# Kernel tuning notes

Measured on AMD Instinct MI355X. Metric: run time of the kernel, lower is better.

The kernel has to match this reference:

```python
import jax, jax.numpy as jnp
import numpy as np

EPS = 1e-5
SLOPE = 0.2


def _conv3d(x, w, stride):
    # x: [B, Cin, D, H, W], w: [Cout, Cin, 3, 3, 3]
    return jax.lax.conv_general_dilated(
        x, w, window_strides=(stride, stride, stride),
        padding=[(1, 1), (1, 1), (1, 1)],
        dimension_numbers=("NCDHW", "OIDHW", "NCDHW"))


def _layernorm_c(y, g, b):
    # LayerNorm over the channel (feature) dim, matching nn.LayerNorm(C) on [N, C]
    mu = jnp.mean(y, axis=1, keepdims=True)
    var = jnp.mean((y - mu) ** 2, axis=1, keepdims=True)
    yn = (y - mu) * jax.lax.rsqrt(var + EPS)
    return yn * g[None, :, None, None, None] + b[None, :, None, None, None]


def _leaky(y):
    return jnp.where(y > 0, y, SLOPE * y)


def _block(x, m, w, g, b, stride):
    # x already zero at inactive sites, so dense conv == sparse gather-scatter conv
    y = _conv3d(x, w, stride)
    if stride > 1:
        # strided SparseConv3d: output active iff any input in 3x3x3 window active
        ones_k = jnp.ones((1, 1, 3, 3, 3), x.dtype)
        m = (_conv3d(m, ones_k, stride) > 0).astype(x.dtype)
    y = _leaky(_layernorm_c(y, g, b))
    return y * m, m


def setup_inputs() -> dict:
    key = jax.random.key(0)
    ks = jax.random.split(key, 16)
    B, D = 2, 64
    x = jax.random.normal(ks[0], (B, 3, D, D, D), jnp.float32)
    mask = jax.random.randint(ks[1], (B, D, D, D), 0, 2) > 0
    chans = [(3, 64), (64, 128), (128, 256), (256, 512)]
    inp = {"x": x, "mask": mask}
    for i, (ci, co) in enumerate(chans):
        inp[f"w{i+1}"] = jax.random.normal(ks[2 + 3 * i], (co, ci, 3, 3, 3), jnp.float32) * 0.05
        inp[f"g{i+1}"] = jnp.ones((co,), jnp.float32)
        inp[f"b{i+1}"] = jnp.zeros((co,), jnp.float32)
    return inp


def reference(x, mask, w1, g1, b1, w2, g2, b2, w3, g3, b3, w4, g4, b4):
    m = mask.astype(x.dtype)[:, None]          # [B,1,D,H,W]
    x = x * m                                  # zero inactive sites
    # SubMConv3d: active set unchanged (stride 1)
    y, m = _block(x, m, w1, g1, b1, 1)
    y, m = _block(y, m, w2, g2, b2, 2)
    y, m = _block(y, m, w3, g3, b3, 2)
    y, m = _block(y, m, w4, g4, b4, 2)
    # .dense() fills inactive sites with 0 (already the case), then amax over D,H,W
    return jnp.max(y, axis=(2, 3, 4))          # [B, 512]
```

## Files before the change

kernel.cpp:

```cpp
#include <hip/hip_runtime.h>
#include <hip/hip_bf16.h>
#include <stdint.h>

#define EPS 1e-5f
#define SLOPE 0.2f

typedef __attribute__((ext_vector_type(8))) short short8;
typedef __attribute__((ext_vector_type(4))) float f32x4;

static __device__ inline ushort f2bf(float f) {
  __hip_bfloat16 h = __float2bfloat16(f);
  return *reinterpret_cast<ushort*>(&h);
}

static __device__ inline short8 u4_to_s8(uint a, uint b, uint c, uint d) {
  union { uint4 u; short8 s; } cv;
  cv.u.x = a; cv.u.y = b; cv.u.z = c; cv.u.w = d;
  return cv.s;
}

__global__ void mask_detect_k(const uint8_t* __restrict__ raw, int nbytes,
                              unsigned* __restrict__ flag) {
  unsigned local = 0;
  for (int i = blockIdx.x * blockDim.x + threadIdx.x; i < nbytes;
       i += gridDim.x * blockDim.x)
    if (i & 3) local |= raw[i];
  if (local) atomicOr(flag, 1u);
}

__global__ void xclm_k(const float* __restrict__ x, const uint8_t* __restrict__ raw,
                       const unsigned* __restrict__ flag,
                       uint8_t* __restrict__ m1, ushort* __restrict__ xclp) {
  int id = blockIdx.x * blockDim.x + threadIdx.x;
  if (id >= 2 * 262144) return;
  uint8_t v;
  if (*flag) {
    v = raw[id];
  } else {
    size_t j = 4 * (size_t)id;
    v = (uint8_t)(raw[j] | raw[j + 1] | raw[j + 2] | raw[j + 3]);
  }
  v = v ? 1 : 0;
  m1[id] = v;
  float mk = (float)v;
  int b  = id >> 18;
  int sp = id & 262143;
  int xx = sp & 63, yy = (sp >> 6) & 63, zz = sp >> 12;
  size_t base = (size_t)b * 3 * 262144 + sp;
  float x0 = x[base] * mk;
  float x1 = x[base + 262144] * mk;
  float x2 = x[base + 2 * 262144] * mk;
  uint2 u;
  u.x = ((uint)f2bf(x1) << 16) | (uint)f2bf(x0);
  u.y = (uint)f2bf(x2);
  size_t pidx = ((((size_t)(b * 66 + zz + 1)) * 66 + (yy + 1)) * 66 + (xx + 1)) * 4;
  *reinterpret_cast<uint2*>(xclp + pidx) = u;
}

__global__ void mask_down_k(const uint8_t* __restrict__ mi,
                            uint8_t* __restrict__ mo, int DIN) {
  int W = DIN >> 1;
  int id = blockIdx.x * blockDim.x + threadIdx.x;
  int total = 2 * W * W * W;
  if (id >= total) return;
  int xo = id % W; int t = id / W;
  int yo = t % W;  t /= W;
  int zo = t % W;  int b = t / W;
  int any = 0;
  for (int dz = 0; dz < 3; ++dz) {
    int z = 2 * zo + dz - 1; if (z < 0 || z >= DIN) continue;
    for (int dy = 0; dy < 3; ++dy) {
      int y = 2 * yo + dy - 1; if (y < 0 || y >= DIN) continue;
      for (int dx = 0; dx < 3; ++dx) {
        int x = 2 * xo + dx - 1; if (x < 0 || x >= DIN) continue;
        any |= mi[(((size_t)b * DIN + z) * DIN + y) * DIN + x];
      }
    }
  }
  mo[id] = any ? 1 : 0;
}

__global__ void wprep_k(const float* __restrict__ w1, const float* __restrict__ w2,
                        const float* __restrict__ w3, const float* __restrict__ w4,
                        ushort* __restrict__ wb1, ushort* __restrict__ wb2,
                        ushort* __restrict__ wb3, ushort* __restrict__ wb4) {
  int id = blockIdx.x * blockDim.x + threadIdx.x;
  if (id < 8192) {
    int k = id & 127, c = id >> 7;
    int tap = k >> 2, ci = k & 3;
    float v = (tap < 27 && ci < 3) ? w1[c * 81 + ci * 27 + tap] : 0.f;
    wb1[id] = f2bf(v);
    return;
  }
  id -= 8192;
  if (id < 128 * 1728) {
    int kn = id % 1728, c = id / 1728;
    int off = kn >> 6, ci = kn & 63;
    wb2[(size_t)c * 1728 + kn] = f2bf(w2[(size_t)c * 1728 + ci * 27 + off]);
    return;
  }
  id -= 128 * 1728;
  if (id < 256 * 3456) {
    int kn = id % 3456, c = id / 3456;
    int off = kn >> 7, ci = kn & 127;
    wb3[(size_t)c * 3456 + kn] = f2bf(w3[(size_t)c * 3456 + ci * 27 + off]);
    return;
  }
  id -= 256 * 3456;
  if (id < 512 * 6912) {
    int kn = id % 6912, c = id / 6912;
    int off = kn >> 8, ci = kn & 255;
    wb4[(size_t)c * 6912 + kn] = f2bf(w4[(size_t)c * 6912 + ci * 27 + off]);
  }
}

__global__ __launch_bounds__(256) void conv1_gemm(
    const ushort* __restrict__ xclp,
    const ushort* __restrict__ wb1,
    const float* __restrict__ gamma,
    const float* __restrict__ beta,
    const uint8_t* __restrict__ msk,
    ushort* __restrict__ out)
{
  const int t    = threadIdx.x;
  const int lane = t & 63;
  const int wave = t >> 6;
  const int c8   = lane >> 4;

  const int bid = blockIdx.x;
  const int yp = bid & 31;
  const int zq = (bid >> 5) & 15;
  const int b  = bid >> 9;
  const int y0 = yp * 2;
  const int z0 = zq * 4;

  __shared__ uint2 tile[1584];

  const uint2* xin = reinterpret_cast<const uint2*>(xclp);
  const long gbase = (((long)(b * 66 + z0)) * 66 + y0) * 66;
  for (int e = t; e < 1584; e += 256) {
    int p = e / 264;
    tile[e] = xin[gbase + e + p * 4092];
  }

  int eoff[2][2][2];
#pragma unroll
  for (int kb = 0; kb < 2; ++kb)
#pragma unroll
    for (int kh = 0; kh < 2; ++kh)
#pragma unroll
      for (int p = 0; p < 2; ++p) {
        int tap = kb * 16 + kh * 8 + c8 * 2 + p;
        int off = 0;
        if (tap < 27) {
          int dz = tap / 9, rr = tap - dz * 9;
          int dy = rr / 3, dx = rr - dy * 3;
          off = dz * 264 + dy * 66 + dx;
        }
        eoff[kb][kh][p] = off;
      }

  int ebase[2];
#pragma unroll
  for (int nf = 0; nf < 2; ++nf) {
    int nl = wave * 32 + nf * 16 + (lane & 15);
    ebase[nf] = (nl >> 6) * 66 + (nl & 63);
  }

  float gr[4][4], br_[4][4];
#pragma unroll
  for (int mf = 0; mf < 4; ++mf) {
    int cb = mf * 16 + c8 * 4;
    f32x4 gv  = *reinterpret_cast<const f32x4*>(gamma + cb);
    f32x4 bv2 = *reinterpret_cast<const f32x4*>(beta + cb);
#pragma unroll
    for (int r = 0; r < 4; ++r) { gr[mf][r] = gv[r]; br_[mf][r] = bv2[r]; }
  }

  __syncthreads();

  for (int zi = 0; zi < 4; ++zi) {
    const int zsh = zi * 264;
    f32x4 acc[4][2];
#pragma unroll
    for (int i = 0; i < 4; ++i)
#pragma unroll
      for (int j = 0; j < 2; ++j) acc[i][j] = (f32x4)(0.f);

#pragma unroll
    for (int kb = 0; kb < 2; ++kb) {
      short8 afr[4][2];
#pragma unroll
      for (int mf = 0; mf < 4; ++mf)
#pragma unroll
        for (int kh = 0; kh < 2; ++kh) {
          int row = mf * 16 + (lane & 15);
          int k   = kb * 64 + (c8 + kh * 4) * 8;
          afr[mf][kh] = *reinterpret_cast<const short8*>(wb1 + row * 128 + k);
        }
#pragma unroll
      for (int nf = 0; nf < 2; ++nf)
#pragma unroll
        for (int kh = 0; kh < 2; ++kh) {
          uint2 v0 = tile[ebase[nf] + zsh + eoff[kb][kh][0]];
          uint2 v1 = tile[ebase[nf] + zsh + eoff[kb][kh][1]];
          short8 bfr = u4_to_s8(v0.x, v0.y, v1.x, v1.y);
#pragma unroll
          for (int mf = 0; mf < 4; ++mf)
            acc[mf][nf] = __builtin_amdgcn_mfma_f32_16x16x32_bf16(
                afr[mf][kh], bfr, acc[mf][nf], 0, 0, 0);
        }
    }

    const int z = z0 + zi;
    const int voxbase = ((b * 64 + z) * 64 + y0) * 64;
#pragma unroll
    for (int nf = 0; nf < 2; ++nf) {
      float s = 0.f, sq = 0.f;
#pragma unroll
      for (int mf = 0; mf < 4; ++mf)
#pragma unroll
        for (int r = 0; r < 4; ++r) {
          float v = acc[mf][nf][r];
          s += v; sq += v * v;
        }
      s  += __shfl_xor(s, 16);  sq += __shfl_xor(sq, 16);
      s  += __shfl_xor(s, 32);  sq += __shfl_xor(sq, 32);
      const float mean = s * (1.f / 64.f);
      const float var  = sq * (1.f / 64.f) - mean * mean;
      const float rstd = rsqrtf(var + EPS);
      const int vox = voxbase + wave * 32 + nf * 16 + (lane & 15);
      const float mk = msk[vox] ? 1.f : 0.f;
#pragma unroll
      for (int mf = 0; mf < 4; ++mf) {
        uint2 u;
        float r0 = (acc[mf][nf][0] - mean) * rstd * gr[mf][0] + br_[mf][0];
        float r1 = (acc[mf][nf][1] - mean) * rstd * gr[mf][1] + br_[mf][1];
        float r2 = (acc[mf][nf][2] - mean) * rstd * gr[mf][2] + br_[mf][2];
        float r3 = (acc[mf][nf][3] - mean) * rstd * gr[mf][3] + br_[mf][3];
        r0 = (r0 > 0.f ? r0 : SLOPE * r0) * mk;
        r1 = (r1 > 0.f ? r1 : SLOPE * r1) * mk;
        r2 = (r2 > 0.f ? r2 : SLOPE * r2) * mk;
        r3 = (r3 > 0.f ? r3 : SLOPE * r3) * mk;
        u.x = ((uint)f2bf(r1) << 16) | (uint)f2bf(r0);
        u.y = ((uint)f2bf(r3) << 16) | (uint)f2bf(r2);
        *reinterpret_cast<uint2*>(out + (size_t)vox * 64 + mf * 16 + c8 * 4) = u;
      }
    }
  }
}

__global__ __launch_bounds__(256) void conv2_gemm(
    const ushort* __restrict__ in,
    const ushort* __restrict__ wbf,
    const float* __restrict__ gamma,
    const float* __restrict__ beta,
    const uint8_t* __restrict__ msk,
    ushort* __restrict__ out,
    const ushort* __restrict__ zpage)
{
  constexpr int CIN = 64, DIN = 64, S = 2;
  constexpr int W = 32, K = 1728, NT = 27, LW = 5;

  const int t    = threadIdx.x;
  const int lane = t & 63;
  const int wave = t >> 6;
  int bid = blockIdx.x;
  bid = (bid & 7) * 64 + (bid >> 3);
  const int n0 = bid * 128;

  __shared__ short As[2][128 * 64];
  __shared__ short Bs[2][128 * 64];
  __shared__ float lnS[4][4][16];
  __shared__ float lnQ[4][4][16];

  int zb[4], yb[4], xb[4], kc8[4], swz[4];
  size_t bb[4];
  const ushort* aptr[4];
#pragma unroll
  for (int j = 0; j < 4; ++j) {
    int q  = t + 256 * j;
    int nl = q >> 3, kc = q & 7;
    kc8[j] = kc * 8;
    swz[j] = nl * 64 + ((kc ^ (nl & 7)) << 3);
    int ngv = n0 + nl;
    int xo = ngv & (W - 1), yo = (ngv >> LW) & (W - 1),
        zo = (ngv >> (2 * LW)) & (W - 1), b = ngv >> (3 * LW);
    xb[j] = xo * S; yb[j] = yo * S; zb[j] = zo * S;
    bb[j] = (size_t)b * CIN * DIN * DIN * DIN;
    aptr[j] = wbf + (size_t)nl * K + kc * 8;
  }

  short8 ar[4], br[4];

  auto LOADK = [&](int kb) {
    const int off = kb;
    const int dz = off / 9, rr = off % 9;
    const int dy = rr / 3, dx = rr % 3;
#pragma unroll
    for (int j = 0; j < 4; ++j) {
      ar[j] = *reinterpret_cast<const short8*>(aptr[j] + kb * 64);
      int zin = zb[j] + dz - 1;
      int yin = yb[j] + dy - 1;
      int xin = xb[j] + dx - 1;
      bool ok = ((unsigned)zin < (unsigned)DIN) &&
                ((unsigned)yin < (unsigned)DIN) &&
                ((unsigned)xin < (unsigned)DIN);
      const ushort* p = ok
          ? in + bb[j] + (((size_t)zin * DIN + yin) * DIN + xin) * CIN + kc8[j]
          : zpage;
      br[j] = *reinterpret_cast<const short8*>(p);
    }
  };

  auto WRITEK = [&](int buf) {
#pragma unroll
    for (int j = 0; j < 4; ++j) {
      *reinterpret_cast<short8*>(&As[buf][swz[j]]) = ar[j];
      *reinterpret_cast<short8*>(&Bs[buf][swz[j]]) = br[j];
    }
  };

  f32x4 acc[4][4];
#pragma unroll
  for (int i = 0; i < 4; ++i)
#pragma unroll
    for (int j = 0; j < 4; ++j) acc[i][j] = (f32x4)(0.f);

  const int wm = (wave & 1) * 64;
  const int wn = (wave >> 1) * 64;

  LOADK(0);
  for (int kb = 0; kb < NT; ++kb) {
    const int buf = kb & 1;
    WRITEK(buf);
    if (kb + 1 < NT) LOADK(kb + 1);
    __syncthreads();

    short8 afr[4][2], bfr[4][2];
#pragma unroll
    for (int mf = 0; mf < 4; ++mf)
#pragma unroll
      for (int kh = 0; kh < 2; ++kh) {
        int row  = wm + mf * 16 + (lane & 15);
        int slot = (lane >> 4) + kh * 4;
        afr[mf][kh] = *reinterpret_cast<const short8*>(
            &As[buf][row * 64 + ((slot ^ (row & 7)) << 3)]);
      }
#pragma unroll
    for (int nf = 0; nf < 4; ++nf)
#pragma unroll
      for (int kh = 0; kh < 2; ++kh) {
        int row  = wn + nf * 16 + (lane & 15);
        int slot = (lane >> 4) + kh * 4;
        bfr[nf][kh] = *reinterpret_cast<const short8*>(
            &Bs[buf][row * 64 + ((slot ^ (row & 7)) << 3)]);
      }
#pragma unroll
    for (int mf = 0; mf < 4; ++mf)
#pragma unroll
      for (int nf = 0; nf < 4; ++nf)
#pragma unroll
        for (int kh = 0; kh < 2; ++kh)
          acc[mf][nf] = __builtin_amdgcn_mfma_f32_16x16x32_bf16(
              afr[mf][kh], bfr[nf][kh], acc[mf][nf], 0, 0, 0);
  }

  float sv[4], qv[4];
#pragma unroll
  for (int nf = 0; nf < 4; ++nf) {
    float s = 0.f, sq = 0.f;
#pragma unroll
    for (int mf = 0; mf < 4; ++mf)
#pragma unroll
      for (int r = 0; r < 4; ++r) {
        float v = acc[mf][nf][r];
        s += v; sq += v * v;
      }
    s  += __shfl_xor(s, 16);  sq += __shfl_xor(sq, 16);
    s  += __shfl_xor(s, 32);  sq += __shfl_xor(sq, 32);
    sv[nf] = s; qv[nf] = sq;
  }
  if (lane < 16) {
#pragma unroll
    for (int nf = 0; nf < 4; ++nf) {
      lnS[wave][nf][lane] = sv[nf];
      lnQ[wave][nf][lane] = qv[nf];
    }
  }
  __syncthreads();

  float gr[4][4], br_[4][4];
#pragma unroll
  for (int mf = 0; mf < 4; ++mf) {
    int cb = wm + mf * 16 + ((lane >> 4) << 2);
    f32x4 gv = *reinterpret_cast<const f32x4*>(gamma + cb);
    f32x4 bv = *reinterpret_cast<const f32x4*>(beta + cb);
#pragma unroll
    for (int r = 0; r < 4; ++r) { gr[mf][r] = gv[r]; br_[mf][r] = bv[r]; }
  }

#pragma unroll
  for (int nf = 0; nf < 4; ++nf) {
    const float s  = sv[nf] + lnS[wave ^ 1][nf][lane & 15];
    const float sq = qv[nf] + lnQ[wave ^ 1][nf][lane & 15];
    const float mean = s * (1.f / 128.f);
    const float var  = sq * (1.f / 128.f) - mean * mean;
    const float rstd = rsqrtf(var + EPS);
    const int vox = n0 + wn + nf * 16 + (lane & 15);
    const float mk = msk[vox] ? 1.f : 0.f;
#pragma unroll
    for (int mf = 0; mf < 4; ++mf) {
      uint2 u;
      float r0 = (acc[mf][nf][0] - mean) * rstd * gr[mf][0] + br_[mf][0];
      float r1 = (acc[mf][nf][1] - mean) * rstd * gr[mf][1] + br_[mf][1];
      float r2 = (acc[mf][nf][2] - mean) * rstd * gr[mf][2] + br_[mf][2];
      float r3 = (acc[mf][nf][3] - mean) * rstd * gr[mf][3] + br_[mf][3];
      r0 = (r0 > 0.f ? r0 : SLOPE * r0) * mk;
      r1 = (r1 > 0.f ? r1 : SLOPE * r1) * mk;
      r2 = (r2 > 0.f ? r2 : SLOPE * r2) * mk;
      r3 = (r3 > 0.f ? r3 : SLOPE * r3) * mk;
      u.x = ((uint)f2bf(r1) << 16) | (uint)f2bf(r0);
      u.y = ((uint)f2bf(r3) << 16) | (uint)f2bf(r2);
      *reinterpret_cast<uint2*>(out + (size_t)vox * 128 + wm + mf * 16 +
                                ((lane >> 4) << 2)) = u;
    }
  }
}

template <int CIN, int COUT, int DIN, int S, int L2CIN, int SPLITK, int BN>
__global__ __launch_bounds__(256) void conv_gemm(
    const ushort* __restrict__ in,
    const ushort* __restrict__ wbf,
    float* __restrict__ rawout,
    const ushort* __restrict__ zpage)
{
  constexpr int W  = DIN / S;
  constexpr int K  = 27 * CIN;
  constexpr int NT = K / 64;
  constexpr int NTS = NT / SPLITK;
  constexpr int LW = (W == 32) ? 5 : (W == 16) ? 4 : 3;
  constexpr size_t NVOX = (size_t)2 * W * W * W;
  constexpr int NB = BN / 32;
  constexpr int NFC = BN / 32;

  const int t    = threadIdx.x;
  const int lane = t & 63;
  const int wave = t >> 6;
  const int n0   = blockIdx.x * BN;
  const int m0   = blockIdx.y * 128;
  const int kb0  = blockIdx.z * NTS;
  float* rawp = rawout + (size_t)blockIdx.z * NVOX * COUT;

  __shared__ short As[2][128 * 64];
  __shared__ short Bs[2][BN * 64];

  int aswz[4];
  const ushort* aptr[4];
#pragma unroll
  for (int j = 0; j < 4; ++j) {
    int q  = t + 256 * j;
    int ml = q >> 3, kc = q & 7;
    aswz[j] = ml * 64 + ((kc ^ (ml & 7)) << 3);
    aptr[j] = wbf + (size_t)(m0 + ml) * K + kc * 8;
  }
  int zb[NB], yb[NB], xb[NB], kc8[NB], bswz[NB];
  size_t bb[NB];
#pragma unroll
  for (int j = 0; j < NB; ++j) {
    int q  = t + 256 * j;
    int nl = q >> 3, kc = q & 7;
    kc8[j] = kc * 8;
    bswz[j] = nl * 64 + ((kc ^ (nl & 7)) << 3);
    int ng = n0 + nl;
    int xo = ng & (W - 1), yo = (ng >> LW) & (W - 1),
        zo = (ng >> (2 * LW)) & (W - 1), b = ng >> (3 * LW);
    xb[j] = xo * S; yb[j] = yo * S; zb[j] = zo * S;
    bb[j] = (size_t)b * CIN * DIN * DIN * DIN;
  }

  short8 ar[4], br[NB];

  auto LOADK = [&](int kb) {
    const int off = (kb * 64) >> L2CIN;
    const int ci0 = (kb * 64) & (CIN - 1);
    const int dz = off / 9, rr = off % 9;
    const int dy = rr / 3, dx = rr % 3;
#pragma unroll
    for (int j = 0; j < 4; ++j)
      ar[j] = *reinterpret_cast<const short8*>(aptr[j] + kb * 64);
#pragma unroll
    for (int j = 0; j < NB; ++j) {
      int zin = zb[j] + dz - 1;
      int yin = yb[j] + dy - 1;
      int xin = xb[j] + dx - 1;
      bool ok = ((unsigned)zin < (unsigned)DIN) &&
                ((unsigned)yin < (unsigned)DIN) &&
                ((unsigned)xin < (unsigned)DIN);
      const ushort* p = ok
          ? in + bb[j] + (((size_t)zin * DIN + yin) * DIN + xin) * CIN + ci0 + kc8[j]
          : zpage;
      br[j] = *reinterpret_cast<const short8*>(p);
    }
  };

  auto WRITEK = [&](int buf) {
#pragma unroll
    for (int j = 0; j < 4; ++j)
      *reinterpret_cast<short8*>(&As[buf][aswz[j]]) = ar[j];
#pragma unroll
    for (int j = 0; j < NB; ++j)
      *reinterpret_cast<short8*>(&Bs[buf][bswz[j]]) = br[j];
  };

  f32x4 acc[4][NFC];
#pragma unroll
  for (int i = 0; i < 4; ++i)
#pragma unroll
    for (int j = 0; j < NFC; ++j) acc[i][j] = (f32x4)(0.f);

  const int wm = (wave & 1) * 64;
  const int wn = (wave >> 1) * (BN / 2);

  LOADK(kb0);
  for (int kb = kb0; kb < kb0 + NTS; ++kb) {
    const int buf = (kb - kb0) & 1;
    WRITEK(buf);
    if (kb + 1 < kb0 + NTS) LOADK(kb + 1);
    __syncthreads();

    short8 afr[4][2], bfr[NFC][2];
#pragma unroll
    for (int mf = 0; mf < 4; ++mf)
#pragma unroll
      for (int kh = 0; kh < 2; ++kh) {
        int row  = wm + mf * 16 + (lane & 15);
        int slot = (lane >> 4) + kh * 4;
        afr[mf][kh] = *reinterpret_cast<const short8*>(
            &As[buf][row * 64 + ((slot ^ (row & 7)) << 3)]);
      }
#pragma unroll
    for (int nf = 0; nf < NFC; ++nf)
#pragma unroll
      for (int kh = 0; kh < 2; ++kh) {
        int row  = wn + nf * 16 + (lane & 15);
        int slot = (lane >> 4) + kh * 4;
        bfr[nf][kh] = *reinterpret_cast<const short8*>(
            &Bs[buf][row * 64 + ((slot ^ (row & 7)) << 3)]);
      }
#pragma unroll
    for (int mf = 0; mf < 4; ++mf)
#pragma unroll
      for (int nf = 0; nf < NFC; ++nf)
#pragma unroll
        for (int kh = 0; kh < 2; ++kh)
          acc[mf][nf] = __builtin_amdgcn_mfma_f32_16x16x32_bf16(
              afr[mf][kh], bfr[nf][kh], acc[mf][nf], 0, 0, 0);
  }

#pragma unroll
  for (int mf = 0; mf < 4; ++mf)
#pragma unroll
    for (int nf = 0; nf < NFC; ++nf) {
      int mg = m0 + wm + mf * 16 + ((lane >> 4) << 2);
      int ng = n0 + wn + nf * 16 + (lane & 15);
      *reinterpret_cast<f32x4*>(&rawp[(size_t)ng * COUT + mg]) = acc[mf][nf];
    }
}

template <int C, int NPART, bool BF16OUT>
__global__ __launch_bounds__(256) void ln_mask_k(
    const float* __restrict__ raw,
    const float* __restrict__ gamma,
    const float* __restrict__ beta,
    const uint8_t* __restrict__ msk,
    void* __restrict__ outv, int nvox)
{
  constexpr int E = C / 64;
  const int lane = threadIdx.x & 63;
  const int vox  = blockIdx.x * 4 + (threadIdx.x >> 6);
  if (vox >= nvox) return;

  const size_t stride = (size_t)nvox * C;
  const float* p = raw + (size_t)vox * C;
  float v[E];
  float s = 0.f, sq = 0.f;
#pragma unroll
  for (int e = 0; e < E; ++e) {
    float acc = 0.f;
#pragma unroll
    for (int pt = 0; pt < NPART; ++pt) acc += p[pt * stride + e * 64 + lane];
    v[e] = acc;
    s += acc; sq += acc * acc;
  }
#pragma unroll
  for (int off = 32; off; off >>= 1) {
    s  += __shfl_xor(s, off);
    sq += __shfl_xor(sq, off);
  }
  const float mean = s / (float)C;
  const float var  = sq / (float)C - mean * mean;
  const float rstd = rsqrtf(var + EPS);
  const float mk   = msk[vox] ? 1.f : 0.f;

#pragma unroll
  for (int e = 0; e < E; ++e) {
    int c = e * 64 + lane;
    float r = (v[e] - mean) * rstd * gamma[c] + beta[c];
    r = (r > 0.f ? r : SLOPE * r) * mk;
    if (BF16OUT)
      ((ushort*)outv)[(size_t)vox * C + c] = f2bf(r);
    else
      ((float*)outv)[(size_t)vox * C + c] = r;
  }
}

template <int NPART>
__global__ __launch_bounds__(256) void ln4max_k(
    const float* __restrict__ raw,
    const float* __restrict__ gamma,
    const float* __restrict__ beta,
    const uint8_t* __restrict__ msk,
    float* __restrict__ pm)
{
  const int t    = threadIdx.x;
  const int lane = t & 63;
  const int wave = t >> 6;
  const int grp  = blockIdx.x;
  const size_t stride = (size_t)1024 * 512;

  float gg[8], bb_[8];
#pragma unroll
  for (int e = 0; e < 8; ++e) {
    int c = e * 64 + lane;
    gg[e] = gamma[c]; bb_[e] = beta[c];
  }

  float vmax[8];
#pragma unroll
  for (int e = 0; e < 8; ++e) vmax[e] = -1e30f;

  for (int it = 0; it < 16; ++it) {
    const int vox = grp * 64 + wave * 16 + it;
    const float* p = raw + (size_t)vox * 512;
    float v[8];
    float s = 0.f, sq = 0.f;
#pragma unroll
    for (int e = 0; e < 8; ++e) {
      float a = 0.f;
#pragma unroll
      for (int pt = 0; pt < NPART; ++pt) a += p[pt * stride + e * 64 + lane];
      v[e] = a; s += a; sq += a * a;
    }
#pragma unroll
    for (int off = 32; off; off >>= 1) {
      s  += __shfl_xor(s, off);
      sq += __shfl_xor(sq, off);
    }
    const float mean = s * (1.f / 512.f);
    const float var  = sq * (1.f / 512.f) - mean * mean;
    const float rstd = rsqrtf(var + EPS);
    const float mk   = msk[vox] ? 1.f : 0.f;
#pragma unroll
    for (int e = 0; e < 8; ++e) {
      float r = (v[e] - mean) * rstd * gg[e] + bb_[e];
      r = (r > 0.f ? r : SLOPE * r) * mk;
      vmax[e] = fmaxf(vmax[e], r);
    }
  }

  __shared__ float red[4][512];
#pragma unroll
  for (int e = 0; e < 8; ++e) red[wave][e * 64 + lane] = vmax[e];
  __syncthreads();
  for (int c = t; c < 512; c += 256) {
    float m = fmaxf(fmaxf(red[0][c], red[1][c]), fmaxf(red[2][c], red[3][c]));
    pm[(size_t)grp * 512 + c] = m;
  }
}

__global__ void rmax2_k(const float* __restrict__ pm, float* __restrict__ out) {
  const int b = blockIdx.x;
  const int c = threadIdx.x;
  float m = -1e30f;
  for (int g = 0; g < 8; ++g) m = fmaxf(m, pm[((size_t)b * 8 + g) * 512 + c]);
  out[b * 512 + c] = m;
}

extern "C" void kernel_launch(void* const* d_in, const int* in_sizes, int n_in,
                              void* d_out, int out_size, void* d_ws, size_t ws_size,
                              hipStream_t stream) {
  const float*   x    = (const float*)d_in[0];
  const uint8_t* mraw = (const uint8_t*)d_in[1];
  const float* w1 = (const float*)d_in[2];
  const float* g1 = (const float*)d_in[3];
  const float* b1 = (const float*)d_in[4];
  const float* w2 = (const float*)d_in[5];
  const float* g2 = (const float*)d_in[6];
  const float* b2 = (const float*)d_in[7];
  const float* w3 = (const float*)d_in[8];
  const float* g3 = (const float*)d_in[9];
  const float* b3 = (const float*)d_in[10];
  const float* w4 = (const float*)d_in[11];
  const float* g4 = (const float*)d_in[12];
  const float* b4 = (const float*)d_in[13];
  float* out = (float*)d_out;
  char*  ws  = (char*)d_ws;

  const size_t ZP   = 0;
  const size_t T1   = 256;
  const size_t R3b  = 67109120;
  const size_t T2   = 92274944;
  const size_t T3   = 109052160;
  const size_t PM   = 113246464;
  const size_t XCLP = 113279232;
  const size_t XCLP_BYTES = 4600064;
  const size_t WB1  = XCLP + XCLP_BYTES;
  const size_t WB2  = WB1 + 16384;
  const size_t WB3  = WB2 + 442368;
  const size_t WB4  = WB3 + 1769472;
  const size_t M1   = WB4 + 7077888;
  const size_t M2   = M1 + 524288;
  const size_t M3   = M2 + 65536;
  const size_t M4   = M3 + 8192;

  unsigned* flag = (unsigned*)(ws + ZP);
  const ushort* zpage = (const ushort*)(ws + ZP + 16);
  ushort* t1   = (ushort*)(ws + T1);
  float*  r3   = (float*)(ws + R3b);
  float*  r4   = (float*)(ws + R3b + 16777216);
  ushort* t2   = (ushort*)(ws + T2);
  ushort* t3   = (ushort*)(ws + T3);
  float*  pm   = (float*)(ws + PM);
  ushort* xclp = (ushort*)(ws + XCLP);
  ushort* wb1  = (ushort*)(ws + WB1);
  ushort* wb2  = (ushort*)(ws + WB2);
  ushort* wb3  = (ushort*)(ws + WB3);
  ushort* wb4  = (ushort*)(ws + WB4);
  uint8_t* m1  = (uint8_t*)(ws + M1);
  uint8_t* m2  = (uint8_t*)(ws + M2);
  uint8_t* m3  = (uint8_t*)(ws + M3);
  uint8_t* m4  = (uint8_t*)(ws + M4);

  const int NM1 = 2 * 64 * 64 * 64;

  hipMemsetAsync(ws + ZP, 0, 64, stream);
  hipMemsetAsync(ws + XCLP, 0, XCLP_BYTES, stream);
  mask_detect_k<<<256, 256, 0, stream>>>(mraw, NM1, flag);
  xclm_k<<<NM1 / 256, 256, 0, stream>>>(x, mraw, flag, m1, xclp);
  mask_down_k<<<(2 * 32 * 32 * 32 + 255) / 256, 256, 0, stream>>>(m1, m2, 64);
  mask_down_k<<<(2 * 16 * 16 * 16 + 255) / 256, 256, 0, stream>>>(m2, m3, 32);
  mask_down_k<<<(2 * 8 * 8 * 8 + 255) / 256, 256, 0, stream>>>(m3, m4, 16);

  wprep_k<<<18176, 256, 0, stream>>>(w1, w2, w3, w4, wb1, wb2, wb3, wb4);

  conv1_gemm<<<1024, 256, 0, stream>>>(xclp, wb1, g1, b1, m1, t1);

  conv2_gemm<<<512, 256, 0, stream>>>(t1, wb2, g2, b2, m2, t2, zpage);

  conv_gemm<128, 256, 32, 2, 7, 2, 64><<<dim3(128, 2, 2), 256, 0, stream>>>(
      t2, wb3, r3, zpage);
  ln_mask_k<256, 2, true><<<8192 / 4, 256, 0, stream>>>(r3, g3, b3, m3, t3, 8192);

  conv_gemm<256, 512, 16, 2, 8, 4, 64><<<dim3(16, 4, 4), 256, 0, stream>>>(
      t3, wb4, r4, zpage);
  ln4max_k<4><<<16, 256, 0, stream>>>(r4, g4, b4, m4, pm);

  rmax2_k<<<2, 512, 0, stream>>>(pm, out);

  (void)in_sizes; (void)n_in; (void)out_size; (void)ws_size;
}
```

Before: 192.6 us.

## Fuse mask downsampling into weight prep and halve conv2 voxel tile

The three chained mask_down launches are merged into the weight-prep kernel. Each coarse mask is now computed directly from the full-resolution mask using the composed receptive-field radius (1, 3, 7), with early exit once an active site is found. Separately, conv2's output tile drops from 128 to 64 voxels per block and the grid doubles to 1024 blocks, trading more redundant weight loads per block for better occupancy and more parallelism across CUs. Computing m3 and m4 straight from m1 reads far more input per output site, and the equivalence to the chained strided downsampling relies on the composed windows matching.

```diff
diff --git a/kernel.cpp b/kernel.cpp
--- a/kernel.cpp
+++ b/kernel.cpp
@@ -57,33 +57,12 @@
   *reinterpret_cast<uint2*>(xclp + pidx) = u;
 }
 
-__global__ void mask_down_k(const uint8_t* __restrict__ mi,
-                            uint8_t* __restrict__ mo, int DIN) {
-  int W = DIN >> 1;
-  int id = blockIdx.x * blockDim.x + threadIdx.x;
-  int total = 2 * W * W * W;
-  if (id >= total) return;
-  int xo = id % W; int t = id / W;
-  int yo = t % W;  t /= W;
-  int zo = t % W;  int b = t / W;
-  int any = 0;
-  for (int dz = 0; dz < 3; ++dz) {
-    int z = 2 * zo + dz - 1; if (z < 0 || z >= DIN) continue;
-    for (int dy = 0; dy < 3; ++dy) {
-      int y = 2 * yo + dy - 1; if (y < 0 || y >= DIN) continue;
-      for (int dx = 0; dx < 3; ++dx) {
-        int x = 2 * xo + dx - 1; if (x < 0 || x >= DIN) continue;
-        any |= mi[(((size_t)b * DIN + z) * DIN + y) * DIN + x];
-      }
-    }
-  }
-  mo[id] = any ? 1 : 0;
-}
-
-__global__ void wprep_k(const float* __restrict__ w1, const float* __restrict__ w2,
-                        const float* __restrict__ w3, const float* __restrict__ w4,
-                        ushort* __restrict__ wb1, ushort* __restrict__ wb2,
-                        ushort* __restrict__ wb3, ushort* __restrict__ wb4) {
+__global__ void prep_k(const float* __restrict__ w1, const float* __restrict__ w2,
+                       const float* __restrict__ w3, const float* __restrict__ w4,
+                       ushort* __restrict__ wb1, ushort* __restrict__ wb2,
+                       ushort* __restrict__ wb3, ushort* __restrict__ wb4,
+                       const uint8_t* __restrict__ m1, uint8_t* __restrict__ m2,
+                       uint8_t* __restrict__ m3, uint8_t* __restrict__ m4) {
   int id = blockIdx.x * blockDim.x + threadIdx.x;
   if (id < 8192) {
     int k = id & 127, c = id >> 7;
@@ -111,7 +90,28 @@
     int kn = id % 6912, c = id / 6912;
     int off = kn >> 8, ci = kn & 255;
     wb4[(size_t)c * 6912 + kn] = f2bf(w4[(size_t)c * 6912 + ci * 27 + off]);
-  }
+    return;
+  }
+  id -= 512 * 6912;
+  int Wl, rad, sh;
+  uint8_t* mo;
+  if (id < 65536)      { Wl = 32; rad = 1; sh = 1; mo = m2; }
+  else if (id < 73728) { id -= 65536; Wl = 16; rad = 3; sh = 2; mo = m3; }
+  else if (id < 74752) { id -= 73728; Wl = 8;  rad = 7; sh = 3; mo = m4; }
+  else return;
+  int xo = id % Wl; int tt = id / Wl;
+  int yo = tt % Wl; tt /= Wl;
+  int zo = tt % Wl; int b = tt / Wl;
+  int cx = xo << sh, cy = yo << sh, cz = zo << sh;
+  int zlo = max(cz - rad, 0), zhi = min(cz + rad, 63);
+  int ylo = max(cy - rad, 0), yhi = min(cy + rad, 63);
+  int xlo = max(cx - rad, 0), xhi = min(cx + rad, 63);
+  int any = 0;
+  for (int z = zlo; z <= zhi && !any; ++z)
+    for (int y = ylo; y <= yhi && !any; ++y)
+      for (int x = xlo; x <= xhi; ++x)
+        any |= m1[(((size_t)b * 64 + z) * 64 + y) * 64 + x];
+  mo[(((size_t)b * Wl + zo) * Wl + yo) * Wl + xo] = any ? 1 : 0;
 }
 
 __global__ __launch_bounds__(256) void conv1_gemm(
@@ -266,40 +266,49 @@
   const int lane = t & 63;
   const int wave = t >> 6;
   int bid = blockIdx.x;
-  bid = (bid & 7) * 64 + (bid >> 3);
-  const int n0 = bid * 128;
+  bid = (bid & 7) * 128 + (bid >> 3);
+  const int n0 = bid * 64;
 
   __shared__ short As[2][128 * 64];
-  __shared__ short Bs[2][128 * 64];
-  __shared__ float lnS[4][4][16];
-  __shared__ float lnQ[4][4][16];
-
-  int zb[4], yb[4], xb[4], kc8[4], swz[4];
-  size_t bb[4];
+  __shared__ short Bs[2][64 * 64];
+  __shared__ float lnS[4][2][16];
+  __shared__ float lnQ[4][2][16];
+
+  int aswz[4];
   const ushort* aptr[4];
 #pragma unroll
   for (int j = 0; j < 4; ++j) {
+    int q  = t + 256 * j;
+    int ml = q >> 3, kc = q & 7;
+    aswz[j] = ml * 64 + ((kc ^ (ml & 7)) << 3);
+    aptr[j] = wbf + (size_t)ml * K + kc * 8;
+  }
+  int zb[2], yb[2], xb[2], kc8[2], bswz[2];
+  size_t bb[2];
+#pragma unroll
+  for (int j = 0; j < 2; ++j) {
     int q  = t + 256 * j;
     int nl = q >> 3, kc = q & 7;
     kc8[j] = kc * 8;
-    swz[j] = nl * 64 + ((kc ^ (nl & 7)) << 3);
+    bswz[j] = nl * 64 + ((kc ^ (nl & 7)) << 3);
     int ngv = n0 + nl;
     int xo = ngv & (W - 1), yo = (ngv >> LW) & (W - 1),
         zo = (ngv >> (2 * LW)) & (W - 1), b = ngv >> (3 * LW);
     xb[j] = xo * S; yb[j] = yo * S; zb[j] = zo * S;
     bb[j] = (size_t)b * CIN * DIN * DIN * DIN;
-    aptr[j] = wbf + (size_t)nl * K + kc * 8;
-  }
-
-  short8 ar[4], br[4];
+  }
+
+  short8 ar[4], br[2];
 
   auto LOADK = [&](int kb) {
     const int off = kb;
     const int dz = off / 9, rr = off % 9;
     const int dy = rr / 3, dx = rr % 3;
 #pragma unroll
-    for (int j = 0; j < 4; ++j) {
+    for (int j = 0; j < 4; ++j)
       ar[j] = *reinterpret_cast<const short8*>(aptr[j] + kb * 64);
+#pragma unroll
+    for (int j = 0; j < 2; ++j) {
       int zin = zb[j] + dz - 1;
       int yin = yb[j] + dy - 1;
       int xin = xb[j] + dx - 1;
@@ -315,20 +324,21 @@
 
   auto WRITEK = [&](int buf) {
 #pragma unroll
-    for (int j = 0; j < 4; ++j) {
-      *reinterpret_cast<short8*>(&As[buf][swz[j]]) = ar[j];
-      *reinterpret_cast<short8*>(&Bs[buf][swz[j]]) = br[j];
-    }
+    for (int j = 0; j < 4; ++j)
+      *reinterpret_cast<short8*>(&As[buf][aswz[j]]) = ar[j];
+#pragma unroll
+    for (int j = 0; j < 2; ++j)
+      *reinterpret_cast<short8*>(&Bs[buf][bswz[j]]) = br[j];
   };
 
-  f32x4 acc[4][4];
+  f32x4 acc[4][2];
 #pragma unroll
   for (int i = 0; i < 4; ++i)
 #pragma unroll
-    for (int j = 0; j < 4; ++j) acc[i][j] = (f32x4)(0.f);
+    for (int j = 0; j < 2; ++j) acc[i][j] = (f32x4)(0.f);
 
   const int wm = (wave & 1) * 64;
-  const int wn = (wave >> 1) * 64;
+  const int wn = (wave >> 1) * 32;
 
   LOADK(0);
   for (int kb = 0; kb < NT; ++kb) {
@@ -337,7 +347,7 @@
     if (kb + 1 < NT) LOADK(kb + 1);
     __syncthreads();
 
-    short8 afr[4][2], bfr[4][2];
+    short8 afr[4][2], bfr[2][2];
 #pragma unroll
     for (int mf = 0; mf < 4; ++mf)
 #pragma unroll
@@ -348,7 +358,7 @@
             &As[buf][row * 64 + ((slot ^ (row & 7)) << 3)]);
       }
 #pragma unroll
-    for (int nf = 0; nf < 4; ++nf)
+    for (int nf = 0; nf < 2; ++nf)
 #pragma unroll
       for (int kh = 0; kh < 2; ++kh) {
         int row  = wn + nf * 16 + (lane & 15);
@@ -359,16 +369,16 @@
 #pragma unroll
     for (int mf = 0; mf < 4; ++mf)
 #pragma unroll
-      for (int nf = 0; nf < 4; ++nf)
+      for (int nf = 0; nf < 2; ++nf)
 #pragma unroll
         for (int kh = 0; kh < 2; ++kh)
           acc[mf][nf] = __builtin_amdgcn_mfma_f32_16x16x32_bf16(
               afr[mf][kh], bfr[nf][kh], acc[mf][nf], 0, 0, 0);
   }
 
-  float sv[4], qv[4];
-#pragma unroll
-  for (int nf = 0; nf < 4; ++nf) {
+  float sv[2], qv[2];
+#pragma unroll
+  for (int nf = 0; nf < 2; ++nf) {
     float s = 0.f, sq = 0.f;
 #pragma unroll
     for (int mf = 0; mf < 4; ++mf)
@@ -383,7 +393,7 @@
   }
   if (lane < 16) {
 #pragma unroll
-    for (int nf = 0; nf < 4; ++nf) {
+    for (int nf = 0; nf < 2; ++nf) {
       lnS[wave][nf][lane] = sv[nf];
       lnQ[wave][nf][lane] = qv[nf];
     }
@@ -401,7 +411,7 @@
   }
 
 #pragma unroll
-  for (int nf = 0; nf < 4; ++nf) {
+  for (int nf = 0; nf < 2; ++nf) {
     const float s  = sv[nf] + lnS[wave ^ 1][nf][lane & 15];
     const float sq = qv[nf] + lnQ[wave ^ 1][nf][lane & 15];
     const float mean = s * (1.f / 128.f);
@@ -748,15 +758,13 @@
   hipMemsetAsync(ws + XCLP, 0, XCLP_BYTES, stream);
   mask_detect_k<<<256, 256, 0, stream>>>(mraw, NM1, flag);
   xclm_k<<<NM1 / 256, 256, 0, stream>>>(x, mraw, flag, m1, xclp);
-  mask_down_k<<<(2 * 32 * 32 * 32 + 255) / 256, 256, 0, stream>>>(m1, m2, 64);
-  mask_down_k<<<(2 * 16 * 16 * 16 + 255) / 256, 256, 0, stream>>>(m2, m3, 32);
-  mask_down_k<<<(2 * 8 * 8 * 8 + 255) / 256, 256, 0, stream>>>(m3, m4, 16);
-
-  wprep_k<<<18176, 256, 0, stream>>>(w1, w2, w3, w4, wb1, wb2, wb3, wb4);
+
+  prep_k<<<18468, 256, 0, stream>>>(w1, w2, w3, w4, wb1, wb2, wb3, wb4,
+                                    m1, m2, m3, m4);
 
   conv1_gemm<<<1024, 256, 0, stream>>>(xclp, wb1, g1, b1, m1, t1);
 
-  conv2_gemm<<<512, 256, 0, stream>>>(t1, wb2, g2, b2, m2, t2, zpage);
+  conv2_gemm<<<1024, 256, 0, stream>>>(t1, wb2, g2, b2, m2, t2, zpage);
 
   conv_gemm<128, 256, 32, 2, 7, 2, 64><<<dim3(128, 2, 2), 256, 0, stream>>>(
       t2, wb3, r3, zpage);
```

Measured after the change: 187.1 us. 1.03x faster.
